# Performance work log

Hardware: AMD Instinct MI355X
Metric: run time of the kernel (lower is better)

The kernel has to match this reference:

```python
import jax, jax.numpy as jnp
import numpy as np

B, L = 4096, 2048
TAU = 0.85        # DivLoss tau (augmented=True)
MARGIN = 0.0005   # RerankLoss margin
RW = 0.5          # rerank_weight
CW = 0.5          # classi_weight


def setup_inputs() -> dict:
    key = jax.random.key(0)
    k1, k2, k3, k4 = jax.random.split(key, 4)
    # cut_y: per-row probability distribution over L cut positions (softmax output)
    cut_y = jax.nn.softmax(jax.random.normal(k1, (B, L)), axis=1)[..., None]
    # pred_y: sigmoid-like probabilities in (0,1) for BCE
    pred_y = jax.random.uniform(k2, (B, L, 1)) * 0.98 + 0.01
    rerank_y = jax.random.normal(k3, (B, L, 1))
    labels = jax.random.randint(k4, (B, L), 0, 2).astype(jnp.float32)
    return {"pred_y": pred_y, "rerank_y": rerank_y, "cut_y": cut_y, "labels": labels}


def _kl_batchmean(target, log_input):
    # torch.nn.KLDivLoss(reduction='batchmean'): sum(target*(log target - log_input)) / B
    term = jnp.where(target > 0, target * (jnp.log(jnp.where(target > 0, target, 1.0)) - log_input), 0.0)
    return jnp.sum(term) / target.shape[0]


def reference(pred_y, rerank_y, cut_y, labels):
    Bn, Ln = labels.shape
    # ---- DivLoss (metric='f1', div_type='js', augmented=True) ----
    # Vectorized replacement of the per-element double loop:
    # f1 at cut k: p = c/k, r = c/T -> 2*c/(k+T) where c = #relevant in top-k
    c = jnp.cumsum(labels, axis=1)                     # [B,L] prefix relevant counts
    T = c[:, -1:]                                      # [B,1] total relevant per row
    k = jnp.arange(1, Ln + 1, dtype=labels.dtype)      # cut positions 1..L
    r = 2.0 * c / (k[None, :] + T)                     # f1 reward per cut position
    q = jax.nn.softmax(r / TAU, axis=1)                # q = exp(r/tau)/sum
    p = cut_y[..., 0]                                  # output.squeeze()
    log_mean = jnp.log((p + q) * 0.5)
    cutloss = 0.5 * (_kl_batchmean(q, log_mean) + _kl_batchmean(p, log_mean))
    # ---- RerankLoss (hinge on mean pos vs mean neg scores) ----
    s = rerank_y[..., 0]
    pos = (labels == 1.0)
    neg = (labels == 0.0)
    pos_mean = jnp.sum(jnp.where(pos, s, 0.0)) / jnp.sum(pos)
    neg_mean = jnp.sum(jnp.where(neg, s, 0.0)) / jnp.sum(neg)
    rerankloss = jnp.maximum(0.0, neg_mean - pos_mean + MARGIN) * RW
    # ---- BCELoss ----
    pp = pred_y[..., 0]
    bce = -jnp.mean(labels * jnp.log(pp) + (1.0 - labels) * jnp.log(1.0 - pp)) * CW
    return cutloss + rerankloss + bce
```

## Files before the change

### kernel.cpp

```cpp
#include <hip/hip_runtime.h>

namespace {
constexpr int Bn = 4096;
constexpr int Ln = 2048;
constexpr float TAU = 0.85f;
constexpr float MARGIN = 0.0005f;
constexpr float RW = 0.5f;
constexpr float CW = 0.5f;

constexpr int THREADS = 256;
constexpr int EPT = Ln / THREADS;
static_assert(EPT == 8, "layout assumption");

__global__ __launch_bounds__(THREADS) void mt_row_kernel(
    const float* __restrict__ pred,
    const float* __restrict__ rerank,
    const float* __restrict__ cut,
    const float* __restrict__ labels,
    float* __restrict__ part)
{
  const int row  = blockIdx.x;
  const int tid  = threadIdx.x;
  const int lane = tid & 63;
  const int wid  = tid >> 6;
  const size_t base = (size_t)row * Ln + (size_t)tid * EPT;

  __shared__ float wtot[4];
  __shared__ float smid[4][2];
  __shared__ float sacc[4][4];

  const float4 la = *reinterpret_cast<const float4*>(labels + base);
  const float4 lb = *reinterpret_cast<const float4*>(labels + base + 4);
  const float4 ya = *reinterpret_cast<const float4*>(pred   + base);
  const float4 yb = *reinterpret_cast<const float4*>(pred   + base + 4);
  const float4 sa = *reinterpret_cast<const float4*>(rerank + base);
  const float4 sb = *reinterpret_cast<const float4*>(rerank + base + 4);
  const float4 pa = *reinterpret_cast<const float4*>(cut    + base);
  const float4 pb = *reinterpret_cast<const float4*>(cut    + base + 4);

  const float lab[8] = {la.x, la.y, la.z, la.w, lb.x, lb.y, lb.z, lb.w};
  const float y[8]   = {ya.x, ya.y, ya.z, ya.w, yb.x, yb.y, yb.z, yb.w};
  const float sv[8]  = {sa.x, sa.y, sa.z, sa.w, sb.x, sb.y, sb.z, sb.w};
  const float p[8]   = {pa.x, pa.y, pa.z, pa.w, pb.x, pb.y, pb.z, pb.w};

  float bce = 0.f, s_all = 0.f, s_pos = 0.f, plp = 0.f;
  #pragma unroll
  for (int j = 0; j < 8; ++j) {
    const float x = (lab[j] == 1.f) ? y[j] : (1.f - y[j]);
    bce   += __logf(x);
    s_all += sv[j];
    s_pos += sv[j] * lab[j];
    plp   += p[j] * __logf(p[j]);
  }

  float pref[8];
  float run = 0.f;
  #pragma unroll
  for (int j = 0; j < 8; ++j) { run += lab[j]; pref[j] = run; }
  const float own = run;
  float sc = own;
  #pragma unroll
  for (int off = 1; off < 64; off <<= 1) {
    float n = __shfl_up(sc, off, 64);
    if (lane >= off) sc += n;
  }
  if (lane == 63) wtot[wid] = sc;
  __syncthreads();
  float woff = 0.f;
  #pragma unroll
  for (int w = 0; w < 4; ++w) if (w < wid) woff += wtot[w];
  const float T = wtot[0] + wtot[1] + wtot[2] + wtot[3];
  const float excl = woff + sc - own;

  float e[8];
  float esum = 0.f, t1 = 0.f;
  const float kbase = (float)(tid * EPT);
  #pragma unroll
  for (int j = 0; j < 8; ++j) {
    const float c = excl + pref[j];
    const float k = kbase + (float)(j + 1);
    const float z = __fdividef(2.f * c, (k + T) * TAU);
    const float ev = __expf(z);
    e[j] = ev;
    esum += ev;
    t1   += ev * z;
  }
  #pragma unroll
  for (int off = 32; off > 0; off >>= 1) {
    esum += __shfl_xor(esum, off, 64);
    t1   += __shfl_xor(t1,   off, 64);
  }
  if (lane == 0) { smid[wid][0] = esum; smid[wid][1] = t1; }
  __syncthreads();
  esum = smid[0][0] + smid[1][0] + smid[2][0] + smid[3][0];
  t1   = smid[0][1] + smid[1][1] + smid[2][1] + smid[3][1];
  const float inv = 1.f / esum;

  float kl = plp;
  #pragma unroll
  for (int j = 0; j < 8; ++j) {
    const float q  = e[j] * inv;
    const float lm = __logf((p[j] + q) * 0.5f);
    kl -= (p[j] + q) * lm;
  }

  #pragma unroll
  for (int off = 32; off > 0; off >>= 1) {
    kl    += __shfl_xor(kl,    off, 64);
    s_all += __shfl_xor(s_all, off, 64);
    s_pos += __shfl_xor(s_pos, off, 64);
    bce   += __shfl_xor(bce,   off, 64);
  }
  if (lane == 0) { sacc[wid][0] = kl; sacc[wid][1] = s_all; sacc[wid][2] = s_pos; sacc[wid][3] = bce; }
  __syncthreads();
  if (tid == 0) {
    const float klrow = sacc[0][0] + sacc[1][0] + sacc[2][0] + sacc[3][0]
                      + t1 * inv - __logf(esum);
    part[0 * Bn + row] = klrow;
    part[1 * Bn + row] = sacc[0][1] + sacc[1][1] + sacc[2][1] + sacc[3][1];
    part[2 * Bn + row] = sacc[0][2] + sacc[1][2] + sacc[2][2] + sacc[3][2];
    part[3 * Bn + row] = sacc[0][3] + sacc[1][3] + sacc[2][3] + sacc[3][3];
    part[4 * Bn + row] = T;
  }
}

__global__ __launch_bounds__(256) void mt_final_kernel(
    const float* __restrict__ part, float* __restrict__ out)
{
  const int tid  = threadIdx.x;
  const int lane = tid & 63;
  const int wid  = tid >> 6;
  double kl = 0, sv = 0, sp = 0, bc = 0, tt = 0;
  for (int r = tid; r < Bn; r += 256) {
    kl += (double)part[0 * Bn + r];
    sv += (double)part[1 * Bn + r];
    sp += (double)part[2 * Bn + r];
    bc += (double)part[3 * Bn + r];
    tt += (double)part[4 * Bn + r];
  }
  #pragma unroll
  for (int off = 32; off > 0; off >>= 1) {
    kl += __shfl_xor(kl, off, 64);
    sv += __shfl_xor(sv, off, 64);
    sp += __shfl_xor(sp, off, 64);
    bc += __shfl_xor(bc, off, 64);
    tt += __shfl_xor(tt, off, 64);
  }
  __shared__ double sh[4][5];
  if (lane == 0) { sh[wid][0] = kl; sh[wid][1] = sv; sh[wid][2] = sp; sh[wid][3] = bc; sh[wid][4] = tt; }
  __syncthreads();
  if (tid == 0) {
    kl = sh[0][0] + sh[1][0] + sh[2][0] + sh[3][0];
    sv = sh[0][1] + sh[1][1] + sh[2][1] + sh[3][1];
    sp = sh[0][2] + sh[1][2] + sh[2][2] + sh[3][2];
    bc = sh[0][3] + sh[1][3] + sh[2][3] + sh[3][3];
    tt = sh[0][4] + sh[1][4] + sh[2][4] + sh[3][4];
    const double total = (double)Bn * (double)Ln;
    const double posc = tt, negc = total - tt;
    double rer = (sv - sp) / negc - sp / posc + (double)MARGIN;
    if (rer < 0.0) rer = 0.0;
    rer *= (double)RW;
    const double cutl = 0.5 * kl / (double)Bn;
    const double bcel = -(bc / total) * (double)CW;
    out[0] = (float)(cutl + rer + bcel);
  }
}
}

extern "C" void kernel_launch(void* const* d_in, const int* in_sizes, int n_in,
                              void* d_out, int out_size, void* d_ws, size_t ws_size,
                              hipStream_t stream) {
  const float* pred   = (const float*)d_in[0];
  const float* rerank = (const float*)d_in[1];
  const float* cut    = (const float*)d_in[2];
  const float* labels = (const float*)d_in[3];
  float* part = (float*)d_ws;
  mt_row_kernel<<<Bn, THREADS, 0, stream>>>(pred, rerank, cut, labels, part);
  mt_final_kernel<<<1, 256, 0, stream>>>(part, (float*)d_out);
}
```

Before: 155.8 us.

## Assign one wavefront per row to drop shared-memory block synchronisation

Each 64-lane wavefront now handles a whole row of 32 elements per lane, with four rows per block, so the row scan and reductions run entirely through wave shuffles and need no __syncthreads or shared-memory staging. Loads are reordered so the cut tensor is fetched after the BCE and rerank work, which keeps register pressure down. The cost is a much larger per-thread register footprint (several 32-float arrays), which may reduce occupancy. Each lane also reads strided 128-byte chunks, which changes the coalescing pattern.

```diff
diff --git a/kernel.cpp b/kernel.cpp
--- a/kernel.cpp
+++ b/kernel.cpp
@@ -8,80 +8,82 @@
 constexpr float RW = 0.5f;
 constexpr float CW = 0.5f;
 
-constexpr int THREADS = 256;
-constexpr int EPT = Ln / THREADS;
-static_assert(EPT == 8, "layout assumption");
+constexpr int ROWS_PER_BLOCK = 4;
+constexpr int EPL = Ln / 64;
+static_assert(EPL == 32, "layout assumption");
 
-__global__ __launch_bounds__(THREADS) void mt_row_kernel(
+__global__ __launch_bounds__(256) void mt_row_kernel(
     const float* __restrict__ pred,
     const float* __restrict__ rerank,
     const float* __restrict__ cut,
     const float* __restrict__ labels,
     float* __restrict__ part)
 {
-  const int row  = blockIdx.x;
   const int tid  = threadIdx.x;
   const int lane = tid & 63;
   const int wid  = tid >> 6;
-  const size_t base = (size_t)row * Ln + (size_t)tid * EPT;
+  const int row  = blockIdx.x * ROWS_PER_BLOCK + wid;
+  const size_t base = (size_t)row * Ln + (size_t)lane * EPL;
 
-  __shared__ float wtot[4];
-  __shared__ float smid[4][2];
-  __shared__ float sacc[4][4];
-
-  const float4 la = *reinterpret_cast<const float4*>(labels + base);
-  const float4 lb = *reinterpret_cast<const float4*>(labels + base + 4);
-  const float4 ya = *reinterpret_cast<const float4*>(pred   + base);
-  const float4 yb = *reinterpret_cast<const float4*>(pred   + base + 4);
-  const float4 sa = *reinterpret_cast<const float4*>(rerank + base);
-  const float4 sb = *reinterpret_cast<const float4*>(rerank + base + 4);
-  const float4 pa = *reinterpret_cast<const float4*>(cut    + base);
-  const float4 pb = *reinterpret_cast<const float4*>(cut    + base + 4);
-
-  const float lab[8] = {la.x, la.y, la.z, la.w, lb.x, lb.y, lb.z, lb.w};
-  const float y[8]   = {ya.x, ya.y, ya.z, ya.w, yb.x, yb.y, yb.z, yb.w};
-  const float sv[8]  = {sa.x, sa.y, sa.z, sa.w, sb.x, sb.y, sb.z, sb.w};
-  const float p[8]   = {pa.x, pa.y, pa.z, pa.w, pb.x, pb.y, pb.z, pb.w};
-
-  float bce = 0.f, s_all = 0.f, s_pos = 0.f, plp = 0.f;
+  float A[EPL];
   #pragma unroll
-  for (int j = 0; j < 8; ++j) {
-    const float x = (lab[j] == 1.f) ? y[j] : (1.f - y[j]);
-    bce   += __logf(x);
-    s_all += sv[j];
-    s_pos += sv[j] * lab[j];
-    plp   += p[j] * __logf(p[j]);
+  for (int c = 0; c < 8; ++c) {
+    const float4 v = reinterpret_cast<const float4*>(labels + base)[c];
+    A[4*c+0] = v.x; A[4*c+1] = v.y; A[4*c+2] = v.z; A[4*c+3] = v.w;
+  }
+  float Y[EPL];
+  #pragma unroll
+  for (int c = 0; c < 8; ++c) {
+    const float4 v = reinterpret_cast<const float4*>(pred + base)[c];
+    Y[4*c+0] = v.x; Y[4*c+1] = v.y; Y[4*c+2] = v.z; Y[4*c+3] = v.w;
+  }
+  float S[EPL];
+  #pragma unroll
+  for (int c = 0; c < 8; ++c) {
+    const float4 v = reinterpret_cast<const float4*>(rerank + base)[c];
+    S[4*c+0] = v.x; S[4*c+1] = v.y; S[4*c+2] = v.z; S[4*c+3] = v.w;
   }
 
-  float pref[8];
+  float bce = 0.f, s_all = 0.f, s_pos = 0.f;
+  #pragma unroll
+  for (int j = 0; j < EPL; ++j) {
+    const float x = (A[j] == 1.f) ? Y[j] : (1.f - Y[j]);
+    bce   += __logf(x);
+    s_all += S[j];
+    s_pos += S[j] * A[j];
+  }
+
+  float P[EPL];
+  #pragma unroll
+  for (int c = 0; c < 8; ++c) {
+    const float4 v = reinterpret_cast<const float4*>(cut + base)[c];
+    P[4*c+0] = v.x; P[4*c+1] = v.y; P[4*c+2] = v.z; P[4*c+3] = v.w;
+  }
+
   float run = 0.f;
   #pragma unroll
-  for (int j = 0; j < 8; ++j) { run += lab[j]; pref[j] = run; }
+  for (int j = 0; j < EPL; ++j) { run += A[j]; A[j] = run; }
   const float own = run;
+
   float sc = own;
   #pragma unroll
   for (int off = 1; off < 64; off <<= 1) {
-    float n = __shfl_up(sc, off, 64);
+    const float n = __shfl_up(sc, off, 64);
     if (lane >= off) sc += n;
   }
-  if (lane == 63) wtot[wid] = sc;
-  __syncthreads();
-  float woff = 0.f;
+  const float T    = __shfl(sc, 63, 64);
+  const float excl = sc - own;
+
+  float esum = 0.f, t1 = 0.f;
+  const float kT = T;
+  const float kbase = (float)(lane * EPL);
   #pragma unroll
-  for (int w = 0; w < 4; ++w) if (w < wid) woff += wtot[w];
-  const float T = wtot[0] + wtot[1] + wtot[2] + wtot[3];
-  const float excl = woff + sc - own;
-
-  float e[8];
-  float esum = 0.f, t1 = 0.f;
-  const float kbase = (float)(tid * EPT);
-  #pragma unroll
-  for (int j = 0; j < 8; ++j) {
-    const float c = excl + pref[j];
+  for (int j = 0; j < EPL; ++j) {
+    const float c = excl + A[j];
     const float k = kbase + (float)(j + 1);
-    const float z = __fdividef(2.f * c, (k + T) * TAU);
+    const float z = __fdividef(2.f * c, (k + kT) * TAU);
     const float ev = __expf(z);
-    e[j] = ev;
+    A[j] = ev;
     esum += ev;
     t1   += ev * z;
   }
@@ -90,18 +92,14 @@
     esum += __shfl_xor(esum, off, 64);
     t1   += __shfl_xor(t1,   off, 64);
   }
-  if (lane == 0) { smid[wid][0] = esum; smid[wid][1] = t1; }
-  __syncthreads();
-  esum = smid[0][0] + smid[1][0] + smid[2][0] + smid[3][0];
-  t1   = smid[0][1] + smid[1][1] + smid[2][1] + smid[3][1];
   const float inv = 1.f / esum;
 
-  float kl = plp;
+  float kl = 0.f;
   #pragma unroll
-  for (int j = 0; j < 8; ++j) {
-    const float q  = e[j] * inv;
-    const float lm = __logf((p[j] + q) * 0.5f);
-    kl -= (p[j] + q) * lm;
+  for (int j = 0; j < EPL; ++j) {
+    const float q  = A[j] * inv;
+    const float pq = P[j] + q;
+    kl += P[j] * __logf(P[j]) - pq * __logf(pq * 0.5f);
   }
 
   #pragma unroll
@@ -111,15 +109,11 @@
     s_pos += __shfl_xor(s_pos, off, 64);
     bce   += __shfl_xor(bce,   off, 64);
   }
-  if (lane == 0) { sacc[wid][0] = kl; sacc[wid][1] = s_all; sacc[wid][2] = s_pos; sacc[wid][3] = bce; }
-  __syncthreads();
-  if (tid == 0) {
-    const float klrow = sacc[0][0] + sacc[1][0] + sacc[2][0] + sacc[3][0]
-                      + t1 * inv - __logf(esum);
-    part[0 * Bn + row] = klrow;
-    part[1 * Bn + row] = sacc[0][1] + sacc[1][1] + sacc[2][1] + sacc[3][1];
-    part[2 * Bn + row] = sacc[0][2] + sacc[1][2] + sacc[2][2] + sacc[3][2];
-    part[3 * Bn + row] = sacc[0][3] + sacc[1][3] + sacc[2][3] + sacc[3][3];
+  if (lane == 0) {
+    part[0 * Bn + row] = kl + t1 * inv - __logf(esum);
+    part[1 * Bn + row] = s_all;
+    part[2 * Bn + row] = s_pos;
+    part[3 * Bn + row] = bce;
     part[4 * Bn + row] = T;
   }
 }
@@ -175,6 +169,6 @@
   const float* cut    = (const float*)d_in[2];
   const float* labels = (const float*)d_in[3];
   float* part = (float*)d_ws;
-  mt_row_kernel<<<Bn, THREADS, 0, stream>>>(pred, rerank, cut, labels, part);
+  mt_row_kernel<<<Bn / ROWS_PER_BLOCK, 256, 0, stream>>>(pred, rerank, cut, labels, part);
   mt_final_kernel<<<1, 256, 0, stream>>>(part, (float*)d_out);
 }
```

Measured after the change: 162.3 us. 1.04x slower.
